# Kernel optimization log

Measured on AMD Instinct MI355X. Metric: run time of the kernel, lower is better.

The kernel has to match this reference:

```python
import jax, jax.numpy as jnp
import numpy as np

BETA = 0.25  # commitment loss weight (init kwarg)


def setup_inputs() -> dict:
    key = jax.random.key(0)
    k1, k2 = jax.random.split(key)
    z = jax.random.normal(k1, (16, 32, 32, 256), dtype=jnp.float32)
    embedding = jax.random.normal(k2, (8192, 256), dtype=jnp.float32)
    return {"z": z, "embedding": embedding}


def reference(z, embedding):
    # Eval-mode forward of EMAVectorQuantizer (EMA buffer update only runs in training).
    b, h, w, c = z.shape
    zf = z.reshape(-1, c)  # [N, d]
    # Squared L2 distance to every codebook entry: ||z||^2 + ||e||^2 - 2 z.e
    d = (jnp.sum(zf * zf, axis=1, keepdims=True)
         + jnp.sum(embedding * embedding, axis=1)
         - 2.0 * jnp.einsum('nd,kd->nk', zf, embedding))  # [N, n_embed]
    idx = jnp.argmin(d, axis=1)  # [N]
    z_q = embedding[idx].reshape(z.shape)  # codebook gather

    # Commitment loss (z_q is detached in the original)
    diff = BETA * jnp.mean((jax.lax.stop_gradient(z_q) - z) ** 2)

    # Straight-through estimator
    z_q = z + jax.lax.stop_gradient(z_q - z)
    z_q = jnp.transpose(z_q, (0, 3, 1, 2))  # b h w c -> b c h w

    # Perplexity as written in the source: each one-hot row contributes
    # exactly 1*log(1 + 1e-12), so the mean is a constant == exp(-log1p(1e-12)).
    perplexity = jnp.exp(-jnp.log1p(jnp.float32(1e-12)))

    return z_q, diff, idx, perplexity
```

## Files before the change

kernel.cpp:

```cpp
#include <hip/hip_runtime.h>
#include <hip/hip_bf16.h>
#include <hip/hip_fp16.h>

#define N_VEC   16384
#define K_CODES 8192
#define D_DIM   256
#define NSPLIT  8
#define BM      128
#define BN      128

#define ZQ_SIZE  (16*256*32*32)
#define DIFF_OFF ZQ_SIZE
#define IDX_OFF  (ZQ_SIZE + 1)
#define PERP_OFF (ZQ_SIZE + 1 + N_VEC)

#define WS_ENORM 0
#define WS_ZH    65536
#define WS_EH    (WS_ZH + N_VEC * D_DIM * 2)
#define WS_P2    (WS_EH + K_CODES * D_DIM * 2)
#define WS_IDXI  (WS_P2 + NSPLIT * N_VEC * 16)
#define WS_LOSS  (WS_IDXI + N_VEC * 4)

typedef _Float16 f16x8 __attribute__((ext_vector_type(8)));
typedef float    f32x4 __attribute__((ext_vector_type(4)));

__device__ __forceinline__ unsigned long long skey(float s, int c) {
    unsigned u = __float_as_uint(s);
    u ^= (unsigned)((int)u >> 31) | 0x80000000u;
    return ((unsigned long long)u << 13) | (unsigned)c;
}

__device__ __forceinline__ int swz_off(int row, int dloc) {
    return row * 128 + ((((dloc >> 3) ^ (row & 7))) << 4) + ((dloc & 7) << 1);
}

__device__ __forceinline__ void gload16(const void* g, void* l) {
    __builtin_amdgcn_global_load_lds((const __attribute__((address_space(1))) unsigned int*)g,
                                     (__attribute__((address_space(3))) unsigned int*)l,
                                     16, 0, 0);
}

__global__ __launch_bounds__(256) void convert_kernel(const float* __restrict__ Z,
                                                      const float* __restrict__ E,
                                                      char* __restrict__ ws) {
    const int t  = threadIdx.x;
    const int r  = blockIdx.x * 4 + (t >> 6);
    const int d0 = (t & 63) * 4;
    const float* src;
    char* dh;
    int rowl;
    if (r < N_VEC) {
        src  = Z + (size_t)r * D_DIM;
        rowl = r & 127;
        dh = ws + WS_ZH + (size_t)(((r >> 7) * 4) + (d0 >> 6)) * 16384;
    } else {
        const int re = r - N_VEC;
        src  = E + (size_t)re * D_DIM;
        rowl = re & 127;
        dh = ws + WS_EH + (size_t)(((re >> 7) * 4) + (d0 >> 6)) * 16384;
    }
    const float4 v = *reinterpret_cast<const float4*>(src + d0);
    const unsigned h0 = __half_as_ushort(__float2half(v.x));
    const unsigned h1 = __half_as_ushort(__float2half(v.y));
    const unsigned h2 = __half_as_ushort(__float2half(v.z));
    const unsigned h3 = __half_as_ushort(__float2half(v.w));
    uint2 hi;
    hi.x = h0 | (h1 << 16);  hi.y = h2 | (h3 << 16);
    *reinterpret_cast<uint2*>(dh + swz_off(rowl, d0 & 63)) = hi;
}

__global__ __launch_bounds__(256) void enorm_kernel(const float* __restrict__ E,
                                                    float* __restrict__ enorm) {
    const int tid  = threadIdx.x;
    const int lane = tid & 63;
    const int wid  = tid >> 6;
    const int code = blockIdx.x * 4 + wid;
    const float4 v = *reinterpret_cast<const float4*>(E + (size_t)code * D_DIM + lane * 4);
    float s = v.x * v.x + v.y * v.y + v.z * v.z + v.w * v.w;
    #pragma unroll
    for (int off = 32; off; off >>= 1) s += __shfl_down(s, off);
    if (lane == 0) enorm[code] = s;
}

__global__ __launch_bounds__(256, 2) void vq_mfma_kernel(const char* __restrict__ ws_ro,
                                                         ulonglong2* __restrict__ part2) {
    __shared__ short lds[32768];

    const int tid  = threadIdx.x;
    const int lane = tid & 63, wid = tid >> 6;
    const int lane15 = lane & 15, g = lane >> 4;
    const int wm = wid >> 1, wn = wid & 1;
    const int bx = blockIdx.x, ksp = blockIdx.y;
    const int row0 = bx * BM;

    const char* zh = ws_ro + WS_ZH;
    const char* eh = ws_ro + WS_EH;
    const float* enorm = (const float*)(ws_ro + WS_ENORM);

    int aoff[4], boff[4];
    #pragma unroll
    for (int m = 0; m < 4; ++m) {
        const int row = wm * 64 + m * 16 + lane15;
        aoff[m] = (row * 128 + ((g ^ (row & 7)) << 4)) >> 1;
    }
    #pragma unroll
    for (int n = 0; n < 4; ++n) {
        const int col = wn * 64 + n * 16 + lane15;
        boff[n] = ((col * 128 + ((g ^ (col & 7)) << 4)) >> 1) + 8192;
    }

    float bestv[16];
    int   bestc[16];
    #pragma unroll
    for (int i = 0; i < 16; ++i) { bestv[i] = 3.0e38f; bestc[i] = 0; }

    #define STAGE(s_)                                                              \
    do {                                                                           \
        const int s__ = (s_);                                                      \
        const int kt_ = s__ >> 2, dt_ = s__ & 3;                                   \
        const char* sA = zh + (size_t)(bx * 4 + dt_) * 16384 + wid * 4096 + lane * 16; \
        const char* sB = eh + (size_t)((ksp * 8 + kt_) * 4 + dt_) * 16384 + wid * 4096 + lane * 16; \
        short* dA = lds + (s__ & 1) * 16384 + wid * 2048 + lane * 8;               \
        short* dB = dA + 8192;                                                     \
        _Pragma("unroll")                                                          \
        for (int i_ = 0; i_ < 4; ++i_) {                                           \
            gload16(sA + i_ * 1024, dA + i_ * 512);                                \
            gload16(sB + i_ * 1024, dB + i_ * 512);                                \
        }                                                                          \
    } while (0)

    STAGE(0);
    __syncthreads();

    for (int kt = 0; kt < 8; ++kt) {
        const int kofs = ksp * (K_CODES / NSPLIT) + kt * BN;

        float en[4];
        #pragma unroll
        for (int n = 0; n < 4; ++n) en[n] = enorm[kofs + wn * 64 + n * 16 + lane15];

        f32x4 acc[4][4];
        #pragma unroll
        for (int m = 0; m < 4; ++m)
            #pragma unroll
            for (int n = 0; n < 4; ++n)
                #pragma unroll
                for (int q = 0; q < 4; ++q) acc[m][n][q] = 0.0f;

        for (int dt = 0; dt < 4; ++dt) {
            const int s = kt * 4 + dt;
            if (s + 1 < 32) STAGE(s + 1);
            const int cb = (s & 1) * 16384;

            #pragma unroll
            for (int ksub = 0; ksub < 2; ++ksub) {
                f16x8 a[4], b[4];
                const int x = ksub << 5;
                #pragma unroll
                for (int m = 0; m < 4; ++m)
                    a[m] = *reinterpret_cast<const f16x8*>(lds + cb + (aoff[m] ^ x));
                #pragma unroll
                for (int n = 0; n < 4; ++n)
                    b[n] = *reinterpret_cast<const f16x8*>(lds + cb + (boff[n] ^ x));
                #pragma unroll
                for (int m = 0; m < 4; ++m)
                    #pragma unroll
                    for (int n = 0; n < 4; ++n)
                        acc[m][n] = __builtin_amdgcn_mfma_f32_16x16x32_f16(a[m], b[n], acc[m][n], 0, 0, 0);
            }
            __syncthreads();
        }

        #pragma unroll
        for (int m = 0; m < 4; ++m)
            #pragma unroll
            for (int n = 0; n < 4; ++n) {
                const int c = kofs + wn * 64 + n * 16 + lane15;
                #pragma unroll
                for (int q = 0; q < 4; ++q) {
                    const float sc = fmaf(-2.0f, acc[m][n][q], en[n]);
                    const int sl = m * 4 + q;
                    if (sc < bestv[sl]) { bestv[sl] = sc; bestc[sl] = c; }
                }
            }
    }
    #undef STAGE

    unsigned long long* t2 = reinterpret_cast<unsigned long long*>(lds);
    #pragma unroll
    for (int sl = 0; sl < 16; ++sl) {
        const int m = sl >> 2, q = sl & 3;
        const unsigned long long k1 = skey(bestv[sl], bestc[sl]);
        unsigned long long m1 = k1;
        #pragma unroll
        for (int msk = 1; msk < 16; msk <<= 1) {
            const unsigned long long o = __shfl_xor(m1, msk);
            m1 = (o < m1) ? o : m1;
        }
        unsigned long long k2 = (k1 == m1) ? ~0ull : k1;
        #pragma unroll
        for (int msk = 1; msk < 16; msk <<= 1) {
            const unsigned long long o = __shfl_xor(k2, msk);
            k2 = (o < k2) ? o : k2;
        }
        if (lane15 == 0) {
            const int row64 = m * 16 + g * 4 + q;
            t2[(wid * 64 + row64) * 2 + 0] = m1;
            t2[(wid * 64 + row64) * 2 + 1] = k2;
        }
    }
    __syncthreads();
    if (tid < 128) {
        const int wm2 = tid >> 6, r64 = tid & 63;
        const unsigned long long a1 = t2[((wm2 * 2 + 0) * 64 + r64) * 2 + 0];
        const unsigned long long a2 = t2[((wm2 * 2 + 0) * 64 + r64) * 2 + 1];
        const unsigned long long b1 = t2[((wm2 * 2 + 1) * 64 + r64) * 2 + 0];
        const unsigned long long b2 = t2[((wm2 * 2 + 1) * 64 + r64) * 2 + 1];
        const unsigned long long r1 = (a1 < b1) ? a1 : b1;
        const unsigned long long hi = (a1 < b1) ? b1 : a1;
        const unsigned long long l2 = (a2 < b2) ? a2 : b2;
        const unsigned long long r2 = (hi < l2) ? hi : l2;
        ulonglong2 res;  res.x = r1;  res.y = r2;
        part2[(size_t)ksp * N_VEC + row0 + tid] = res;
    }
}

__global__ __launch_bounds__(256) void rescore_kernel(const float* __restrict__ Z,
                                                      const float* __restrict__ E,
                                                      const ulonglong2* __restrict__ part2,
                                                      int* __restrict__ idx_i,
                                                      float* __restrict__ out_idx) {
    const int tid = threadIdx.x, lane = tid & 63, wid = tid >> 6;
    const int r = blockIdx.x * 4 + wid;
    int c0 = 0, c1 = 0, c2 = 0, c3 = 0;
    if (lane == 0) {
        unsigned long long m0 = ~0ull, m1 = ~0ull, m2 = ~0ull, m3 = ~0ull;
        for (int s = 0; s < NSPLIT; ++s) {
            const ulonglong2 p = part2[(size_t)s * N_VEC + r];
            unsigned long long k = p.x;
            if (k < m0) { m3 = m2; m2 = m1; m1 = m0; m0 = k; }
            else if (k < m1) { m3 = m2; m2 = m1; m1 = k; }
            else if (k < m2) { m3 = m2; m2 = k; }
            else if (k < m3) { m3 = k; }
            k = p.y;
            if (k < m0) { m3 = m2; m2 = m1; m1 = m0; m0 = k; }
            else if (k < m1) { m3 = m2; m2 = m1; m1 = k; }
            else if (k < m2) { m3 = m2; m2 = k; }
            else if (k < m3) { m3 = k; }
        }
        c0 = (int)(m0 & 0x1FFFull);  c1 = (int)(m1 & 0x1FFFull);
        c2 = (int)(m2 & 0x1FFFull);  c3 = (int)(m3 & 0x1FFFull);
    }
    c0 = __shfl(c0, 0);  c1 = __shfl(c1, 0);
    c2 = __shfl(c2, 0);  c3 = __shfl(c3, 0);
    const float4 z4 = *reinterpret_cast<const float4*>(Z + (size_t)r * D_DIM + lane * 4);
    double d[4];
    const int cc[4] = {c0, c1, c2, c3};
    #pragma unroll
    for (int j = 0; j < 4; ++j) {
        const float4 e4 = *reinterpret_cast<const float4*>(E + (size_t)cc[j] * D_DIM + lane * 4);
        const double ax = (double)z4.x - (double)e4.x, ay = (double)z4.y - (double)e4.y;
        const double az = (double)z4.z - (double)e4.z, aw = (double)z4.w - (double)e4.w;
        d[j] = ax * ax + ay * ay + az * az + aw * aw;
    }
    #pragma unroll
    for (int off = 1; off < 64; off <<= 1) {
        #pragma unroll
        for (int j = 0; j < 4; ++j) d[j] += __shfl_xor(d[j], off);
    }
    if (lane == 0) {
        double bd = d[0];  int bi = c0;
        #pragma unroll
        for (int j = 1; j < 4; ++j) {
            if (d[j] < bd || (d[j] == bd && cc[j] < bi)) { bd = d[j]; bi = cc[j]; }
        }
        idx_i[r]   = bi;
        out_idx[r] = (float)bi;
    }
}

__global__ __launch_bounds__(256) void gather_kernel(const float* __restrict__ Z,
                                                     const float* __restrict__ E,
                                                     const int* __restrict__ idx_i,
                                                     float* __restrict__ out,
                                                     float* __restrict__ partials) {
    __shared__ float Ls[128 * 65];
    __shared__ int   sIdx[64];
    __shared__ float red[4];

    const int tid = threadIdx.x;
    const int gb  = blockIdx.x;
    const int n0  = gb * 64;
    const int b   = n0 >> 10;
    const int hwbase = n0 & 1023;

    if (tid < 64) sIdx[tid] = idx_i[n0 + tid];
    __syncthreads();

    float sq = 0.0f;
    {
        const int c4   = tid & 63;
        const int rsub = tid >> 6;
        #pragma unroll
        for (int p = 0; p < 16; ++p) {
            const int r = p * 4 + rsub;
            const float4 z4 = *reinterpret_cast<const float4*>(Z + (size_t)(n0 + r) * D_DIM + c4 * 4);
            const float4 e4 = *reinterpret_cast<const float4*>(E + (size_t)sIdx[r] * D_DIM + c4 * 4);
            const float dx = e4.x - z4.x, dy = e4.y - z4.y, dz = e4.z - z4.z, dw = e4.w - z4.w;
            sq += dx * dx + dy * dy + dz * dz + dw * dw;
        }
    }
    #pragma unroll
    for (int off = 32; off; off >>= 1) sq += __shfl_down(sq, off);
    if ((tid & 63) == 0) red[tid >> 6] = sq;
    __syncthreads();
    if (tid == 0) partials[gb] = red[0] + red[1] + red[2] + red[3];

    for (int h = 0; h < 2; ++h) {
        __syncthreads();
        const int rowl = tid >> 2;
        const int qs   = tid & 3;
        const float* erow = E + (size_t)sIdx[rowl] * D_DIM + h * 128;
        #pragma unroll
        for (int m = 0; m < 8; ++m) {
            const int c4 = m * 4 + qs;
            const float4 v = *reinterpret_cast<const float4*>(erow + c4 * 4);
            Ls[(c4 * 4 + 0) * 65 + rowl] = v.x;
            Ls[(c4 * 4 + 1) * 65 + rowl] = v.y;
            Ls[(c4 * 4 + 2) * 65 + rowl] = v.z;
            Ls[(c4 * 4 + 3) * 65 + rowl] = v.w;
        }
        __syncthreads();
        const int wl   = tid & 63;
        const int csub = tid >> 6;
        #pragma unroll
        for (int pc = 0; pc < 32; ++pc) {
            const int c_l = pc * 4 + csub;
            const int c   = h * 128 + c_l;
            out[((size_t)(b * 256 + c)) * 1024 + hwbase + wl] = Ls[c_l * 65 + wl];
        }
    }
}

__global__ __launch_bounds__(256) void final_kernel(const float* __restrict__ partials,
                                                    float* __restrict__ out) {
    __shared__ float red[4];
    const int tid = threadIdx.x;
    float s = partials[tid];
    #pragma unroll
    for (int off = 32; off; off >>= 1) s += __shfl_down(s, off);
    if ((tid & 63) == 0) red[tid >> 6] = s;
    __syncthreads();
    if (tid == 0) {
        const float total = red[0] + red[1] + red[2] + red[3];
        out[DIFF_OFF] = 0.25f * (total / (float)(N_VEC * D_DIM));
        out[PERP_OFF] = 1.0f;
    }
}

extern "C" void kernel_launch(void* const* d_in, const int* in_sizes, int n_in,
                              void* d_out, int out_size, void* d_ws, size_t ws_size,
                              hipStream_t stream) {
    const float* Z = (const float*)d_in[0];
    const float* E = (const float*)d_in[1];
    float* out = (float*)d_out;
    char*  ws  = (char*)d_ws;

    float*      enorm    = (float*)(ws + WS_ENORM);
    ulonglong2* part2    = (ulonglong2*)(ws + WS_P2);
    int*        idx_i    = (int*)(ws + WS_IDXI);
    float*      lossbuf  = (float*)(ws + WS_LOSS);

    hipLaunchKernelGGL(convert_kernel, dim3((N_VEC + K_CODES) / 4), dim3(256), 0, stream, Z, E, ws);
    hipLaunchKernelGGL(enorm_kernel, dim3(K_CODES / 4), dim3(256), 0, stream, E, enorm);
    hipLaunchKernelGGL(vq_mfma_kernel, dim3(N_VEC / BM, NSPLIT), dim3(256), 0, stream,
                       (const char*)ws, part2);
    hipLaunchKernelGGL(rescore_kernel, dim3(N_VEC / 4), dim3(256), 0, stream,
                       Z, E, part2, idx_i, out + IDX_OFF);
    hipLaunchKernelGGL(gather_kernel, dim3(N_VEC / 64), dim3(256), 0, stream,
                       Z, E, idx_i, out, lossbuf);
    hipLaunchKernelGGL(final_kernel, dim3(1), dim3(256), 0, stream, lossbuf, out);
}
```

Baseline: 128.1 us.

## Keep Z tile in registers, halve K-splits, fuse enorm and loss into other kernels

The distance GEMM kernel now loads each block's 128-row Z tile once into registers (32 f16x8 per lane) and streams only codebook tiles through LDS. This halves LDS usage and the per-stage global loads, and NSPLIT drops from 8 to 4, so each block covers 16 code tiles. The enorm computation moves into convert_kernel, and the commitment-loss partials now come from the rescore kernel's best distance. This removes a launch and a second pass over Z and E in gather. In exchange, the MFMA kernel carries much higher register pressure, which may hurt occupancy, and the grid has fewer blocks.

Result: slower. 245.9 us (+91.9%).

```diff
diff --git a/kernel.cpp b/kernel.cpp
--- a/kernel.cpp
+++ b/kernel.cpp
@@ -5,7 +5,8 @@
 #define N_VEC   16384
 #define K_CODES 8192
 #define D_DIM   256
-#define NSPLIT  8
+#define NSPLIT  4
+#define KT_PER  16
 #define BM      128
 #define BN      128
 
@@ -49,7 +50,8 @@
     const float* src;
     char* dh;
     int rowl;
-    if (r < N_VEC) {
+    const bool isE = (r >= N_VEC);
+    if (!isE) {
         src  = Z + (size_t)r * D_DIM;
         rowl = r & 127;
         dh = ws + WS_ZH + (size_t)(((r >> 7) * 4) + (d0 >> 6)) * 16384;
@@ -67,24 +69,18 @@
     uint2 hi;
     hi.x = h0 | (h1 << 16);  hi.y = h2 | (h3 << 16);
     *reinterpret_cast<uint2*>(dh + swz_off(rowl, d0 & 63)) = hi;
-}
-
-__global__ __launch_bounds__(256) void enorm_kernel(const float* __restrict__ E,
-                                                    float* __restrict__ enorm) {
-    const int tid  = threadIdx.x;
-    const int lane = tid & 63;
-    const int wid  = tid >> 6;
-    const int code = blockIdx.x * 4 + wid;
-    const float4 v = *reinterpret_cast<const float4*>(E + (size_t)code * D_DIM + lane * 4);
-    float s = v.x * v.x + v.y * v.y + v.z * v.z + v.w * v.w;
-    #pragma unroll
-    for (int off = 32; off; off >>= 1) s += __shfl_down(s, off);
-    if (lane == 0) enorm[code] = s;
+
+    if (isE) {
+        float s = v.x * v.x + v.y * v.y + v.z * v.z + v.w * v.w;
+        #pragma unroll
+        for (int off = 32; off; off >>= 1) s += __shfl_down(s, off);
+        if ((t & 63) == 0) ((float*)(ws + WS_ENORM))[r - N_VEC] = s;
+    }
 }
 
 __global__ __launch_bounds__(256, 2) void vq_mfma_kernel(const char* __restrict__ ws_ro,
                                                          ulonglong2* __restrict__ part2) {
-    __shared__ short lds[32768];
+    __shared__ short lds[16384];
 
     const int tid  = threadIdx.x;
     const int lane = tid & 63, wid = tid >> 6;
@@ -97,16 +93,38 @@
     const char* eh = ws_ro + WS_EH;
     const float* enorm = (const float*)(ws_ro + WS_ENORM);
 
-    int aoff[4], boff[4];
-    #pragma unroll
-    for (int m = 0; m < 4; ++m) {
-        const int row = wm * 64 + m * 16 + lane15;
-        aoff[m] = (row * 128 + ((g ^ (row & 7)) << 4)) >> 1;
-    }
+    #define STAGE_B(kt_, dt_)                                                          \
+    do {                                                                               \
+        const char* sB = eh + (size_t)(((ksp * KT_PER + (kt_)) * 4) + (dt_)) * 16384   \
+                            + wid * 4096 + lane * 16;                                  \
+        short* dB = lds + ((dt_) & 1) * 8192 + wid * 2048 + lane * 8;                  \
+        _Pragma("unroll")                                                              \
+        for (int i_ = 0; i_ < 4; ++i_) gload16(sB + i_ * 1024, dB + i_ * 512);         \
+    } while (0)
+
+    STAGE_B(0, 0);
+
+    f16x8 areg[8][4];
+    #pragma unroll
+    for (int dt = 0; dt < 4; ++dt) {
+        const char* tileA = zh + (size_t)(bx * 4 + dt) * 16384;
+        #pragma unroll
+        for (int ksub = 0; ksub < 2; ++ksub)
+            #pragma unroll
+            for (int m = 0; m < 4; ++m) {
+                const int row  = wm * 64 + m * 16 + lane15;
+                const int slot = (ksub * 4 + g) ^ (row & 7);
+                areg[dt * 2 + ksub][m] =
+                    *reinterpret_cast<const f16x8*>(tileA + row * 128 + (slot << 4));
+            }
+    }
+
+    int bbase[4], bx7[4];
     #pragma unroll
     for (int n = 0; n < 4; ++n) {
         const int col = wn * 64 + n * 16 + lane15;
-        boff[n] = ((col * 128 + ((g ^ (col & 7)) << 4)) >> 1) + 8192;
+        bbase[n] = col * 64;
+        bx7[n]   = col & 7;
     }
 
     float bestv[16];
@@ -114,30 +132,10 @@
     #pragma unroll
     for (int i = 0; i < 16; ++i) { bestv[i] = 3.0e38f; bestc[i] = 0; }
 
-    #define STAGE(s_)                                                              \
-    do {                                                                           \
-        const int s__ = (s_);                                                      \
-        const int kt_ = s__ >> 2, dt_ = s__ & 3;                                   \
-        const char* sA = zh + (size_t)(bx * 4 + dt_) * 16384 + wid * 4096 + lane * 16; \
-        const char* sB = eh + (size_t)((ksp * 8 + kt_) * 4 + dt_) * 16384 + wid * 4096 + lane * 16; \
-        short* dA = lds + (s__ & 1) * 16384 + wid * 2048 + lane * 8;               \
-        short* dB = dA + 8192;                                                     \
-        _Pragma("unroll")                                                          \
-        for (int i_ = 0; i_ < 4; ++i_) {                                           \
-            gload16(sA + i_ * 1024, dA + i_ * 512);                                \
-            gload16(sB + i_ * 1024, dB + i_ * 512);                                \
-        }                                                                          \
-    } while (0)
-
-    STAGE(0);
-    __syncthreads();
-
-    for (int kt = 0; kt < 8; ++kt) {
+    __syncthreads();
+
+    for (int kt = 0; kt < KT_PER; ++kt) {
         const int kofs = ksp * (K_CODES / NSPLIT) + kt * BN;
-
-        float en[4];
-        #pragma unroll
-        for (int n = 0; n < 4; ++n) en[n] = enorm[kofs + wn * 64 + n * 16 + lane15];
 
         f32x4 acc[4][4];
         #pragma unroll
@@ -147,26 +145,26 @@
                 #pragma unroll
                 for (int q = 0; q < 4; ++q) acc[m][n][q] = 0.0f;
 
+        #pragma unroll
         for (int dt = 0; dt < 4; ++dt) {
-            const int s = kt * 4 + dt;
-            if (s + 1 < 32) STAGE(s + 1);
-            const int cb = (s & 1) * 16384;
+            if (dt < 3)            STAGE_B(kt, dt + 1);
+            else if (kt < KT_PER - 1) STAGE_B(kt + 1, 0);
+            const int cb = (dt & 1) * 8192;
 
             #pragma unroll
             for (int ksub = 0; ksub < 2; ++ksub) {
-                f16x8 a[4], b[4];
-                const int x = ksub << 5;
+                f16x8 b[4];
                 #pragma unroll
-                for (int m = 0; m < 4; ++m)
-                    a[m] = *reinterpret_cast<const f16x8*>(lds + cb + (aoff[m] ^ x));
-                #pragma unroll
-                for (int n = 0; n < 4; ++n)
-                    b[n] = *reinterpret_cast<const f16x8*>(lds + cb + (boff[n] ^ x));
+                for (int n = 0; n < 4; ++n) {
+                    const int slot = (ksub * 4 + g) ^ bx7[n];
+                    b[n] = *reinterpret_cast<const f16x8*>(lds + cb + bbase[n] + (slot << 3));
+                }
                 #pragma unroll
                 for (int m = 0; m < 4; ++m)
                     #pragma unroll
                     for (int n = 0; n < 4; ++n)
-                        acc[m][n] = __builtin_amdgcn_mfma_f32_16x16x32_f16(a[m], b[n], acc[m][n], 0, 0, 0);
+                        acc[m][n] = __builtin_amdgcn_mfma_f32_16x16x32_f16(
+                            areg[dt * 2 + ksub][m], b[n], acc[m][n], 0, 0, 0);
             }
             __syncthreads();
         }
@@ -175,16 +173,17 @@
         for (int m = 0; m < 4; ++m)
             #pragma unroll
             for (int n = 0; n < 4; ++n) {
-                const int c = kofs + wn * 64 + n * 16 + lane15;
+                const int c  = kofs + wn * 64 + n * 16 + lane15;
+                const float en = enorm[c];
                 #pragma unroll
                 for (int q = 0; q < 4; ++q) {
-                    const float sc = fmaf(-2.0f, acc[m][n][q], en[n]);
+                    const float sc = fmaf(-2.0f, acc[m][n][q], en);
                     const int sl = m * 4 + q;
                     if (sc < bestv[sl]) { bestv[sl] = sc; bestc[sl] = c; }
                 }
             }
     }
-    #undef STAGE
+    #undef STAGE_B
 
     unsigned long long* t2 = reinterpret_cast<unsigned long long*>(lds);
     #pragma unroll
@@ -229,7 +228,9 @@
                                                       const float* __restrict__ E,
                                                       const ulonglong2* __restrict__ part2,
                                                       int* __restrict__ idx_i,
-                                                      float* __restrict__ out_idx) {
+                                                      float* __restrict__ out_idx,
+                                                      float* __restrict__ lossp) {
+    __shared__ double redl[4];
     const int tid = threadIdx.x, lane = tid & 63, wid = tid >> 6;
     const int r = blockIdx.x * 4 + wid;
     int c0 = 0, c1 = 0, c2 = 0, c3 = 0;
@@ -276,17 +277,17 @@
         }
         idx_i[r]   = bi;
         out_idx[r] = (float)bi;
-    }
-}
-
-__global__ __launch_bounds__(256) void gather_kernel(const float* __restrict__ Z,
-                                                     const float* __restrict__ E,
+        redl[wid]  = bd;
+    }
+    __syncthreads();
+    if (tid == 0) lossp[blockIdx.x] = (float)(redl[0] + redl[1] + redl[2] + redl[3]);
+}
+
+__global__ __launch_bounds__(256) void gather_kernel(const float* __restrict__ E,
                                                      const int* __restrict__ idx_i,
-                                                     float* __restrict__ out,
-                                                     float* __restrict__ partials) {
+                                                     float* __restrict__ out) {
     __shared__ float Ls[128 * 65];
     __shared__ int   sIdx[64];
-    __shared__ float red[4];
 
     const int tid = threadIdx.x;
     const int gb  = blockIdx.x;
@@ -297,27 +298,8 @@
     if (tid < 64) sIdx[tid] = idx_i[n0 + tid];
     __syncthreads();
 
-    float sq = 0.0f;
-    {
-        const int c4   = tid & 63;
-        const int rsub = tid >> 6;
-        #pragma unroll
-        for (int p = 0; p < 16; ++p) {
-            const int r = p * 4 + rsub;
-            const float4 z4 = *reinterpret_cast<const float4*>(Z + (size_t)(n0 + r) * D_DIM + c4 * 4);
-            const float4 e4 = *reinterpret_cast<const float4*>(E + (size_t)sIdx[r] * D_DIM + c4 * 4);
-            const float dx = e4.x - z4.x, dy = e4.y - z4.y, dz = e4.z - z4.z, dw = e4.w - z4.w;
-            sq += dx * dx + dy * dy + dz * dz + dw * dw;
-        }
-    }
-    #pragma unroll
-    for (int off = 32; off; off >>= 1) sq += __shfl_down(sq, off);
-    if ((tid & 63) == 0) red[tid >> 6] = sq;
-    __syncthreads();
-    if (tid == 0) partials[gb] = red[0] + red[1] + red[2] + red[3];
-
     for (int h = 0; h < 2; ++h) {
-        __syncthreads();
+        if (h) __syncthreads();
         const int rowl = tid >> 2;
         const int qs   = tid & 3;
         const float* erow = E + (size_t)sIdx[rowl] * D_DIM + h * 128;
@@ -342,11 +324,12 @@
     }
 }
 
-__global__ __launch_bounds__(256) void final_kernel(const float* __restrict__ partials,
+__global__ __launch_bounds__(256) void final_kernel(const float* __restrict__ lossp,
                                                     float* __restrict__ out) {
     __shared__ float red[4];
     const int tid = threadIdx.x;
-    float s = partials[tid];
+    float s = 0.0f;
+    for (int i = tid; i < N_VEC / 4; i += 256) s += lossp[i];
     #pragma unroll
     for (int off = 32; off; off >>= 1) s += __shfl_down(s, off);
     if ((tid & 63) == 0) red[tid >> 6] = s;
@@ -366,18 +349,16 @@
     float* out = (float*)d_out;
     char*  ws  = (char*)d_ws;
 
-    float*      enorm    = (float*)(ws + WS_ENORM);
-    ulonglong2* part2    = (ulonglong2*)(ws + WS_P2);
-    int*        idx_i    = (int*)(ws + WS_IDXI);
-    float*      lossbuf  = (float*)(ws + WS_LOSS);
+    ulonglong2* part2   = (ulonglong2*)(ws + WS_P2);
+    int*        idx_i   = (int*)(ws + WS_IDXI);
+    float*      lossbuf = (float*)(ws + WS_LOSS);
 
     hipLaunchKernelGGL(convert_kernel, dim3((N_VEC + K_CODES) / 4), dim3(256), 0, stream, Z, E, ws);
-    hipLaunchKernelGGL(enorm_kernel, dim3(K_CODES / 4), dim3(256), 0, stream, E, enorm);
     hipLaunchKernelGGL(vq_mfma_kernel, dim3(N_VEC / BM, NSPLIT), dim3(256), 0, stream,
                        (const char*)ws, part2);
     hipLaunchKernelGGL(rescore_kernel, dim3(N_VEC / 4), dim3(256), 0, stream,
-                       Z, E, part2, idx_i, out + IDX_OFF);
+                       Z, E, part2, idx_i, out + IDX_OFF, lossbuf);
     hipLaunchKernelGGL(gather_kernel, dim3(N_VEC / 64), dim3(256), 0, stream,
-                       Z, E, idx_i, out, lossbuf);
+                       E, idx_i, out);
     hipLaunchKernelGGL(final_kernel, dim3(1), dim3(256), 0, stream, lossbuf, out);
 }
```
